# Performance work log

Hardware: AMD Instinct MI355X
Metric: run time of the kernel (lower is better)

## Reference

```python
import jax, jax.numpy as jnp
import numpy as np

D_MODEL = 1024
N_HEADS = 16
HEAD_DIM = D_MODEL // N_HEADS


def setup_inputs() -> dict:
    key = jax.random.key(0)
    k_x, k_q, k_k, k_v = jax.random.split(key, 4)
    B, S = 2, 2048
    x = jax.random.normal(k_x, (B, S, D_MODEL), dtype=jnp.float32)
    # nn.Linear weights stored as [out, in]; we apply x @ W.T
    scale = 1.0 / np.sqrt(D_MODEL)
    W_q = jax.random.uniform(k_q, (D_MODEL, D_MODEL), jnp.float32, -scale, scale)
    W_k = jax.random.uniform(k_k, (D_MODEL, D_MODEL), jnp.float32, -scale, scale)
    W_v = jax.random.uniform(k_v, (D_MODEL, D_MODEL), jnp.float32, -scale, scale)
    return {"x": x, "W_q": W_q, "W_k": W_k, "W_v": W_v}


def reference(x, W_q, W_k, W_v):
    B, S, D = x.shape
    H, Hd = N_HEADS, HEAD_DIM
    # QKV projections (Linear with no bias): x @ W.T
    Q = (x @ W_q.T).reshape(B, S, H, Hd).transpose(0, 2, 1, 3)  # [B,H,S,Hd]
    K = (x @ W_k.T).reshape(B, S, H, Hd).transpose(0, 2, 1, 3)
    V = (x @ W_v.T).reshape(B, S, H, Hd).transpose(0, 2, 1, 3)
    scores = jnp.einsum("bhqd,bhkd->bhqk", Q, K) / jnp.sqrt(jnp.float32(Hd))
    attn = jax.nn.softmax(scores, axis=-1)
    out = jnp.einsum("bhqk,bhkd->bhqd", attn, V)  # [B,H,S,Hd]
    return out.transpose(0, 2, 1, 3).reshape(B, S, H * Hd)
```

## Files before the change

### kernel.cpp

```cpp
#include <hip/hip_runtime.h>
#include <stdint.h>


typedef __bf16 bf16x8 __attribute__((ext_vector_type(8)));
typedef __bf16 bf16x4 __attribute__((ext_vector_type(4)));
typedef __bf16 bf16x2 __attribute__((ext_vector_type(2)));
typedef float  f32x2  __attribute__((ext_vector_type(2)));
typedef float  f32x4  __attribute__((ext_vector_type(4)));
typedef float  f32x16 __attribute__((ext_vector_type(16)));

#define D_MODEL 1024
#define SEQ     2048
#define NHEAD   16
#define HDIM    64
#define BS      4096

__device__ __forceinline__ void load_lds16(const void* g, void* lds) {
  __builtin_amdgcn_global_load_lds(
      (__attribute__((address_space(1))) void*)(uintptr_t)g,
      (__attribute__((address_space(3))) void*)(uintptr_t)lds,
      16, 0, 0);
}

#if __has_builtin(__builtin_amdgcn_exp2f)
#define EXP2F(x) __builtin_amdgcn_exp2f(x)
#else
#define EXP2F(x) __expf(0.6931471805599453f * (x))
#endif

__device__ __forceinline__ uint32_t pack_bf16_pair(float a, float b) {
  f32x2 f = {a, b};
  union { bf16x2 h; uint32_t u; } r;
  r.h = __builtin_convertvector(f, bf16x2);
  return r.u;
}

#define NX4 1048576
#define NW4 262144
__global__ void cvt_all(const float* __restrict__ x,  const float* __restrict__ wq,
                        const float* __restrict__ wk, const float* __restrict__ wv,
                        __bf16* __restrict__ xb,  __bf16* __restrict__ wqb,
                        __bf16* __restrict__ wkb, __bf16* __restrict__ wvb) {
  int i = blockIdx.x * blockDim.x + threadIdx.x;
  const float* in; __bf16* out; int j;
  if (i < NX4)                { in = x;  out = xb;  j = i; }
  else if (i < NX4 + NW4)     { in = wq; out = wqb; j = i - NX4; }
  else if (i < NX4 + 2*NW4)   { in = wk; out = wkb; j = i - NX4 - NW4; }
  else                        { in = wv; out = wvb; j = i - NX4 - 2*NW4; }
  float4 v = ((const float4*)in)[j];
  bf16x4 o;
  o[0] = (__bf16)v.x; o[1] = (__bf16)v.y;
  o[2] = (__bf16)v.z; o[3] = (__bf16)v.w;
  ((bf16x4*)out)[j] = o;
}

__global__ __launch_bounds__(256) void qkv_gemm(
    const __bf16* __restrict__ X,
    const __bf16* __restrict__ Wq, const __bf16* __restrict__ Wk,
    const __bf16* __restrict__ Wv,
    __bf16* __restrict__ Qb, __bf16* __restrict__ Kb, __bf16* __restrict__ Vt) {
  __shared__ __bf16 As[128 * 32];
  __shared__ __bf16 Bs[128 * 32];

  const __bf16* W = (blockIdx.z == 0) ? Wq : (blockIdx.z == 1) ? Wk : Wv;

  const int t    = threadIdx.x;
  const int wv   = t >> 6;
  const int lane = t & 63;
  const int l15  = lane & 15;
  const int quad = lane >> 4;
  const int m0   = blockIdx.y * 128;
  const int n0   = blockIdx.x * 128;
  const int wm   = (wv >> 1) * 64;
  const int wn   = (wv & 1) * 64;

  f32x4 acc[4][4] = {};

  for (int it = 0; it < 32; ++it) {
    const int k0 = it * 32;
#pragma unroll
    for (int p = 0; p < 2; ++p) {
      const int c   = p * 256 + t;
      const int row = c >> 2;
      const int ko  = (c & 3) * 8;
      const unsigned lb = (unsigned)((p * 256 + wv * 64) * 16);
      load_lds16(X + (size_t)(m0 + row) * D_MODEL + k0 + ko, (char*)As + lb);
      load_lds16(W + (size_t)(n0 + row) * D_MODEL + k0 + ko, (char*)Bs + lb);
    }
    __syncthreads();

    bf16x8 af[4], bfb[4];
#pragma unroll
    for (int i = 0; i < 4; ++i)
      af[i] = *(const bf16x8*)&As[(wm + i * 16 + l15) * 32 + quad * 8];
#pragma unroll
    for (int j = 0; j < 4; ++j)
      bfb[j] = *(const bf16x8*)&Bs[(wn + j * 16 + l15) * 32 + quad * 8];
#pragma unroll
    for (int i = 0; i < 4; ++i)
#pragma unroll
      for (int j = 0; j < 4; ++j)
        acc[i][j] = __builtin_amdgcn_mfma_f32_16x16x32_bf16(af[i], bfb[j],
                                                            acc[i][j], 0, 0, 0);
    __syncthreads();
  }

  if (blockIdx.z != 2) {
    __bf16* Out = (blockIdx.z == 0) ? Qb : Kb;
    const float qs = (blockIdx.z == 0) ? 0.125f * 1.4426950408889634f : 1.0f;
#pragma unroll
    for (int i = 0; i < 4; ++i) {
      const int rg = m0 + wm + i * 16 + quad * 4;
#pragma unroll
      for (int j = 0; j < 4; ++j) {
        const int cg = n0 + wn + j * 16 + l15;
#pragma unroll
        for (int r2 = 0; r2 < 4; ++r2)
          Out[(size_t)(rg + r2) * D_MODEL + cg] = (__bf16)(acc[i][j][r2] * qs);
      }
    }
  } else {
#pragma unroll
    for (int i = 0; i < 4; ++i) {
      const int mg = m0 + wm + i * 16 + quad * 4;
#pragma unroll
      for (int j = 0; j < 4; ++j) {
        const int ng = n0 + wn + j * 16 + l15;
        bf16x4 v;
#pragma unroll
        for (int r2 = 0; r2 < 4; ++r2) v[r2] = (__bf16)acc[i][j][r2];
        *(bf16x4*)&Vt[(size_t)ng * BS + mg] = v;
      }
    }
  }
}

__global__ __launch_bounds__(256) void attn(
    const __bf16* __restrict__ Qb, const __bf16* __restrict__ Kb,
    const __bf16* __restrict__ Vt, float* __restrict__ out) {
  __shared__ __align__(16) char smem[16896];
  __bf16* Ks = (__bf16*)smem;
  __bf16* Vs = (__bf16*)(smem + 8192);
  float*  cmb = (float*)smem;

  const int t     = threadIdx.x;
  const int wv    = t >> 6;
  const int qgrp  = wv >> 1;
  const int ktile = wv & 1;
  const int lane  = t & 63;
  const int l31   = lane & 31;
  const int half  = lane >> 5;
  const int h     = blockIdx.y;
  const size_t bo = (size_t)blockIdx.z * SEQ;
  const int q0    = blockIdx.x * 64 + qgrp * 32;
  const int hd0   = h * HDIM;

  bf16x8 qf[4];
#pragma unroll
  for (int c = 0; c < 4; ++c)
    qf[c] = *(const bf16x8*)&Qb[(bo + q0 + l31) * D_MODEL + hd0 + c * 16 + half * 8];

  f32x2 lsum2 = {0.f, 0.f};
  f32x16 o_acc[2] = {};

  const int srow = ktile * 32 + l31;

  for (int kt = 0; kt < SEQ / 64; ++kt) {
    const int n0 = kt * 64;
#pragma unroll
    for (int p = 0; p < 2; ++p) {
      const int c   = p * 256 + t;
      const int row = c >> 3;
      const int cc  = (c & 7) ^ (row & 7);
      const unsigned lb = (unsigned)((p * 256 + wv * 64) * 16);
      load_lds16(Kb + (bo + n0 + row) * D_MODEL + hd0 + cc * 8, (char*)Ks + lb);
      load_lds16(Vt + (size_t)(hd0 + row) * BS + bo + n0 + cc * 8, (char*)Vs + lb);
    }
    __syncthreads();

    f32x16 st = {};
#pragma unroll
    for (int c = 0; c < 4; ++c) {
      const int pc = (2 * c + half) ^ (srow & 7);
      bf16x8 kf = *(const bf16x8*)&Ks[(srow * 8 + pc) * 8];
      st = __builtin_amdgcn_mfma_f32_32x32x16_bf16(kf, qf[c], st, 0, 0, 0);
    }

    uint32_t pk[8];
#pragma unroll
    for (int i = 0; i < 8; ++i) {
      float e0 = EXP2F(st[2 * i]);
      float e1 = EXP2F(st[2 * i + 1]);
      f32x2 e = {e0, e1};
      lsum2 += e;
      pk[i] = pack_bf16_pair(e0, e1);
    }

#pragma unroll
    for (int kc = 0; kc < 2; ++kc) {
      auto r02 = __builtin_amdgcn_permlane32_swap(pk[kc * 4 + 0], pk[kc * 4 + 2],
                                                  false, false);
      auto r13 = __builtin_amdgcn_permlane32_swap(pk[kc * 4 + 1], pk[kc * 4 + 3],
                                                  false, false);
      union { uint32_t u[4]; bf16x8 v; } pf;
      pf.u[0] = r02[0]; pf.u[1] = r13[0];
      pf.u[2] = r02[1]; pf.u[3] = r13[1];
#pragma unroll
      for (int dt = 0; dt < 2; ++dt) {
        const int row = dt * 32 + l31;
        const int pc  = (ktile * 4 + kc * 2 + half) ^ (row & 7);
        bf16x8 vf = *(const bf16x8*)&Vs[(row * 8 + pc) * 8];
        o_acc[dt] = __builtin_amdgcn_mfma_f32_32x32x16_bf16(vf, pf.v,
                                                            o_acc[dt], 0, 0, 0);
      }
    }
    __syncthreads();
  }

  float lsum = lsum2[0] + lsum2[1];

  if (ktile == 1) {
    float* p = cmb + (size_t)(qgrp * 64 + lane) * 33;
#pragma unroll
    for (int dt = 0; dt < 2; ++dt)
#pragma unroll
      for (int g = 0; g < 16; ++g) p[dt * 16 + g] = o_acc[dt][g];
    p[32] = lsum;
  }
  __syncthreads();
  if (ktile == 0) {
    const float* p = cmb + (size_t)(qgrp * 64 + lane) * 33;
#pragma unroll
    for (int dt = 0; dt < 2; ++dt)
#pragma unroll
      for (int g = 0; g < 16; ++g) o_acc[dt][g] += p[dt * 16 + g];
    lsum += p[32];
    lsum += __shfl_xor(lsum, 32);
    const float inv = 1.f / lsum;

    const size_t orow = (bo + q0 + l31) * D_MODEL + hd0;
#pragma unroll
    for (int dt = 0; dt < 2; ++dt)
#pragma unroll
      for (int g = 0; g < 4; ++g) {
        float4 v = make_float4(o_acc[dt][4 * g + 0] * inv, o_acc[dt][4 * g + 1] * inv,
                               o_acc[dt][4 * g + 2] * inv, o_acc[dt][4 * g + 3] * inv);
        *(float4*)&out[orow + dt * 32 + g * 8 + half * 4] = v;
      }
  }
}

extern "C" void kernel_launch(void* const* d_in, const int* in_sizes, int n_in,
                              void* d_out, int out_size, void* d_ws, size_t ws_size,
                              hipStream_t stream) {
  const float* x  = (const float*)d_in[0];
  const float* Wq = (const float*)d_in[1];
  const float* Wk = (const float*)d_in[2];
  const float* Wv = (const float*)d_in[3];
  float* out = (float*)d_out;

  char* ws = (char*)d_ws;
  __bf16* xb  = (__bf16*)(ws);
  __bf16* wqb = (__bf16*)(ws + (8u  << 20));
  __bf16* wkb = (__bf16*)(ws + (10u << 20));
  __bf16* wvb = (__bf16*)(ws + (12u << 20));
  __bf16* Qbf = (__bf16*)(ws + (14u << 20));
  __bf16* Kbf = (__bf16*)(ws + (22u << 20));
  __bf16* Vt  = (__bf16*)(ws + (30u << 20));

  cvt_all<<<(NX4 + 3 * NW4) / 256, 256, 0, stream>>>(x, Wq, Wk, Wv,
                                                     xb, wqb, wkb, wvb);

  qkv_gemm<<<dim3(8, 32, 3), 256, 0, stream>>>(xb, wqb, wkb, wvb, Qbf, Kbf, Vt);

  attn<<<dim3(SEQ / 64, NHEAD, 2), 256, 0, stream>>>(Qbf, Kbf, Vt, out);
}
```

Baseline: 162.3 us.

## Double-buffer K/V tiles in LDS and raise wave priority around MFMAs

The attention loop now uses two LDS buffers, issuing the async global-to-LDS loads for the next K/V tile before computing on the current one, with one vmcnt-wait plus barrier per tile instead of two syncthreads. Address computation is hoisted out of the loop into precomputed per-thread pointers. s_setprio is raised around the MFMA sections to favour matrix issue. The cost is double the LDS footprint, which may lower occupancy, and the single barrier relies on vmcnt ordering being enough to avoid write-after-read hazards on the reused buffer.

```diff
diff --git a/kernel.cpp b/kernel.cpp
--- a/kernel.cpp
+++ b/kernel.cpp
@@ -135,13 +135,17 @@
   }
 }
 
+#define VMBAR do {                                         \
+    asm volatile("s_waitcnt vmcnt(0)" ::: "memory");       \
+    __builtin_amdgcn_s_barrier();                          \
+    asm volatile("" ::: "memory");                         \
+  } while (0)
+
 __global__ __launch_bounds__(256) void attn(
     const __bf16* __restrict__ Qb, const __bf16* __restrict__ Kb,
     const __bf16* __restrict__ Vt, float* __restrict__ out) {
-  __shared__ __align__(16) char smem[16896];
-  __bf16* Ks = (__bf16*)smem;
-  __bf16* Vs = (__bf16*)(smem + 8192);
-  float*  cmb = (float*)smem;
+  __shared__ __align__(16) char smem[32768];
+  float* cmb = (float*)smem;
 
   const int t     = threadIdx.x;
   const int wv    = t >> 6;
@@ -160,31 +164,44 @@
   for (int c = 0; c < 4; ++c)
     qf[c] = *(const bf16x8*)&Qb[(bo + q0 + l31) * D_MODEL + hd0 + c * 16 + half * 8];
 
+  const int row0 = t >> 3;
+  const int row1 = 32 + row0;
+  const int cc0  = (t & 7) ^ (row0 & 7);
+  const int cc1  = (t & 7) ^ (row1 & 7);
+  const __bf16* kp0 = Kb + (bo + row0) * D_MODEL + hd0 + cc0 * 8;
+  const __bf16* kp1 = Kb + (bo + row1) * D_MODEL + hd0 + cc1 * 8;
+  const __bf16* vp0 = Vt + (size_t)(hd0 + row0) * BS + bo + cc0 * 8;
+  const __bf16* vp1 = Vt + (size_t)(hd0 + row1) * BS + bo + cc1 * 8;
+  const unsigned lb0 = (unsigned)(wv * 1024);
+  const unsigned lb1 = (unsigned)(4096 + wv * 1024);
+
   f32x2 lsum2 = {0.f, 0.f};
   f32x16 o_acc[2] = {};
 
   const int srow = ktile * 32 + l31;
 
-  for (int kt = 0; kt < SEQ / 64; ++kt) {
-    const int n0 = kt * 64;
-#pragma unroll
-    for (int p = 0; p < 2; ++p) {
-      const int c   = p * 256 + t;
-      const int row = c >> 3;
-      const int cc  = (c & 7) ^ (row & 7);
-      const unsigned lb = (unsigned)((p * 256 + wv * 64) * 16);
-      load_lds16(Kb + (bo + n0 + row) * D_MODEL + hd0 + cc * 8, (char*)Ks + lb);
-      load_lds16(Vt + (size_t)(hd0 + row) * BS + bo + n0 + cc * 8, (char*)Vs + lb);
-    }
-    __syncthreads();
+  auto stage = [&](char* base, int kt) {
+    const size_t ko = (size_t)kt * (64 * D_MODEL);
+    const int    vo = kt * 64;
+    load_lds16(kp0 + ko, base + lb0);
+    load_lds16(kp1 + ko, base + lb1);
+    load_lds16(vp0 + vo, base + 8192 + lb0);
+    load_lds16(vp1 + vo, base + 8192 + lb1);
+  };
+
+  auto tile_compute = [&](const char* base) {
+    const __bf16* Ks = (const __bf16*)base;
+    const __bf16* Vs = (const __bf16*)(base + 8192);
 
     f32x16 st = {};
+    __builtin_amdgcn_s_setprio(1);
 #pragma unroll
     for (int c = 0; c < 4; ++c) {
       const int pc = (2 * c + half) ^ (srow & 7);
       bf16x8 kf = *(const bf16x8*)&Ks[(srow * 8 + pc) * 8];
       st = __builtin_amdgcn_mfma_f32_32x32x16_bf16(kf, qf[c], st, 0, 0, 0);
     }
+    __builtin_amdgcn_s_setprio(0);
 
     uint32_t pk[8];
 #pragma unroll
@@ -196,6 +213,7 @@
       pk[i] = pack_bf16_pair(e0, e1);
     }
 
+    __builtin_amdgcn_s_setprio(1);
 #pragma unroll
     for (int kc = 0; kc < 2; ++kc) {
       auto r02 = __builtin_amdgcn_permlane32_swap(pk[kc * 4 + 0], pk[kc * 4 + 2],
@@ -214,7 +232,22 @@
                                                             o_acc[dt], 0, 0, 0);
       }
     }
-    __syncthreads();
+    __builtin_amdgcn_s_setprio(0);
+  };
+
+  char* const b0 = smem;
+  char* const b1 = smem + 16384;
+
+  stage(b0, 0);
+  VMBAR;
+
+  for (int kt2 = 0; kt2 < 16; ++kt2) {
+    stage(b1, 2 * kt2 + 1);
+    tile_compute(b0);
+    VMBAR;
+    if (kt2 < 15) stage(b0, 2 * kt2 + 2);
+    tile_compute(b1);
+    VMBAR;
   }
 
   float lsum = lsum2[0] + lsum2[1];
```

New measurement: 162.6 us. No clear change (+0.2%).

## Load K/V fragments directly into registers with double buffering instead of LDS

Applied to the files above, without the earlier changes.

The attention loop no longer stages K and V tiles through shared memory with global_load_lds and two barriers per iteration. Each wave now loads its own K and V MFMA fragments straight from global memory into registers, double-buffered across key tiles so the next tile's loads overlap the current tile's compute. It also raises wave priority with s_setprio around the MFMA blocks. The cost is more registers and more global/L2 traffic, because waves sharing a key tile no longer share the loaded data, and global reads of Vt fragments may be less coalesced.

```diff
diff --git a/kernel.cpp b/kernel.cpp
--- a/kernel.cpp
+++ b/kernel.cpp
@@ -138,10 +138,7 @@
 __global__ __launch_bounds__(256) void attn(
     const __bf16* __restrict__ Qb, const __bf16* __restrict__ Kb,
     const __bf16* __restrict__ Vt, float* __restrict__ out) {
-  __shared__ __align__(16) char smem[16896];
-  __bf16* Ks = (__bf16*)smem;
-  __bf16* Vs = (__bf16*)(smem + 8192);
-  float*  cmb = (float*)smem;
+  __shared__ __align__(16) float cmb[2 * 64 * 33];
 
   const int t     = threadIdx.x;
   const int wv    = t >> 6;
@@ -160,31 +157,33 @@
   for (int c = 0; c < 4; ++c)
     qf[c] = *(const bf16x8*)&Qb[(bo + q0 + l31) * D_MODEL + hd0 + c * 16 + half * 8];
 
+  const int srow = ktile * 32 + l31;
+  const __bf16* kP = Kb + (bo + srow) * D_MODEL + hd0 + half * 8;
+  const __bf16* vP = Vt + (size_t)(hd0 + l31) * BS + bo + ktile * 32 + half * 8;
+
   f32x2 lsum2 = {0.f, 0.f};
   f32x16 o_acc[2] = {};
 
-  const int srow = ktile * 32 + l31;
-
-  for (int kt = 0; kt < SEQ / 64; ++kt) {
-    const int n0 = kt * 64;
-#pragma unroll
-    for (int p = 0; p < 2; ++p) {
-      const int c   = p * 256 + t;
-      const int row = c >> 3;
-      const int cc  = (c & 7) ^ (row & 7);
-      const unsigned lb = (unsigned)((p * 256 + wv * 64) * 16);
-      load_lds16(Kb + (bo + n0 + row) * D_MODEL + hd0 + cc * 8, (char*)Ks + lb);
-      load_lds16(Vt + (size_t)(hd0 + row) * BS + bo + n0 + cc * 8, (char*)Vs + lb);
-    }
-    __syncthreads();
-
+  auto loadt = [&](bf16x8 (&kf)[4], bf16x8 (&vf)[4], int tt) {
+    const __bf16* kp = kP + (size_t)tt * (64 * D_MODEL);
+    const __bf16* vp = vP + tt * 64;
+#pragma unroll
+    for (int c = 0; c < 4; ++c)
+      kf[c] = *(const bf16x8*)(kp + c * 16);
+#pragma unroll
+    for (int kc = 0; kc < 2; ++kc)
+#pragma unroll
+      for (int dt = 0; dt < 2; ++dt)
+        vf[kc * 2 + dt] = *(const bf16x8*)(vp + (size_t)dt * (32 * BS) + kc * 16);
+  };
+
+  auto compute = [&](const bf16x8 (&kf)[4], const bf16x8 (&vf)[4]) {
     f32x16 st = {};
-#pragma unroll
-    for (int c = 0; c < 4; ++c) {
-      const int pc = (2 * c + half) ^ (srow & 7);
-      bf16x8 kf = *(const bf16x8*)&Ks[(srow * 8 + pc) * 8];
-      st = __builtin_amdgcn_mfma_f32_32x32x16_bf16(kf, qf[c], st, 0, 0, 0);
-    }
+    __builtin_amdgcn_s_setprio(1);
+#pragma unroll
+    for (int c = 0; c < 4; ++c)
+      st = __builtin_amdgcn_mfma_f32_32x32x16_bf16(kf[c], qf[c], st, 0, 0, 0);
+    __builtin_amdgcn_s_setprio(0);
 
     uint32_t pk[8];
 #pragma unroll
@@ -196,6 +195,7 @@
       pk[i] = pack_bf16_pair(e0, e1);
     }
 
+    __builtin_amdgcn_s_setprio(1);
 #pragma unroll
     for (int kc = 0; kc < 2; ++kc) {
       auto r02 = __builtin_amdgcn_permlane32_swap(pk[kc * 4 + 0], pk[kc * 4 + 2],
@@ -206,15 +206,20 @@
       pf.u[0] = r02[0]; pf.u[1] = r13[0];
       pf.u[2] = r02[1]; pf.u[3] = r13[1];
 #pragma unroll
-      for (int dt = 0; dt < 2; ++dt) {
-        const int row = dt * 32 + l31;
-        const int pc  = (ktile * 4 + kc * 2 + half) ^ (row & 7);
-        bf16x8 vf = *(const bf16x8*)&Vs[(row * 8 + pc) * 8];
-        o_acc[dt] = __builtin_amdgcn_mfma_f32_32x32x16_bf16(vf, pf.v,
+      for (int dt = 0; dt < 2; ++dt)
+        o_acc[dt] = __builtin_amdgcn_mfma_f32_32x32x16_bf16(vf[kc * 2 + dt], pf.v,
                                                             o_acc[dt], 0, 0, 0);
-      }
-    }
-    __syncthreads();
+    }
+    __builtin_amdgcn_s_setprio(0);
+  };
+
+  bf16x8 ka[4], va[4], kb_[4], vb_[4];
+  loadt(ka, va, 0);
+  for (int kt = 0; kt < 32; kt += 2) {
+    loadt(kb_, vb_, kt + 1);
+    compute(ka, va);
+    if (kt + 2 < 32) loadt(ka, va, kt + 2);
+    compute(kb_, vb_);
   }
 
   float lsum = lsum2[0] + lsum2[1];
```

Result: slower. 228.3 us (+40.7%).

## Split attention KV sweep across four waves per query group with 128-key tiles

Applied to the files above, without the earlier changes.

The attention kernel now launches 512 threads, so each 32-query group is served by four waves that each take a 32-key slice of a 128-key tile, instead of two waves over a 64-key tile. This halves the number of outer-loop iterations and barriers and amortizes the LDS staging over more keys, with precomputed load addresses. In exchange it doubles shared memory per block and adds a two-stage tree reduction of partial outputs across the waves at the end. Higher thread count with a launch-bound hint of 8 may constrain registers.

```diff
diff --git a/kernel.cpp b/kernel.cpp
--- a/kernel.cpp
+++ b/kernel.cpp
@@ -135,18 +135,18 @@
   }
 }
 
-__global__ __launch_bounds__(256) void attn(
+__global__ __launch_bounds__(512, 8) void attn(
     const __bf16* __restrict__ Qb, const __bf16* __restrict__ Kb,
     const __bf16* __restrict__ Vt, float* __restrict__ out) {
-  __shared__ __align__(16) char smem[16896];
+  __shared__ __align__(16) char smem[33792];
   __bf16* Ks = (__bf16*)smem;
-  __bf16* Vs = (__bf16*)(smem + 8192);
+  __bf16* Vs = (__bf16*)(smem + 16384);
   float*  cmb = (float*)smem;
 
   const int t     = threadIdx.x;
   const int wv    = t >> 6;
-  const int qgrp  = wv >> 1;
-  const int ktile = wv & 1;
+  const int qgrp  = wv >> 2;
+  const int ktile = wv & 3;
   const int lane  = t & 63;
   const int l31   = lane & 31;
   const int half  = lane >> 5;
@@ -160,22 +160,28 @@
   for (int c = 0; c < 4; ++c)
     qf[c] = *(const bf16x8*)&Qb[(bo + q0 + l31) * D_MODEL + hd0 + c * 16 + half * 8];
 
+  const int rK = t >> 3;
+  const int cK = (t & 7) ^ (rK & 7);
+  const int rV = t >> 4;
+  const int cV = (t & 15) ^ (rV & 15);
+  const __bf16* kSrc = Kb + (bo + rK) * D_MODEL + hd0 + cK * 8;
+  const __bf16* vSrc = Vt + (size_t)(hd0 + rV) * BS + bo + cV * 8;
+  char* const kDst0 = smem + wv * 1024;
+  char* const kDst1 = smem + 8192 + wv * 1024;
+  char* const vDst0 = smem + 16384 + wv * 1024;
+  char* const vDst1 = smem + 16384 + 8192 + wv * 1024;
+
   f32x2 lsum2 = {0.f, 0.f};
   f32x16 o_acc[2] = {};
 
   const int srow = ktile * 32 + l31;
 
-  for (int kt = 0; kt < SEQ / 64; ++kt) {
-    const int n0 = kt * 64;
-#pragma unroll
-    for (int p = 0; p < 2; ++p) {
-      const int c   = p * 256 + t;
-      const int row = c >> 3;
-      const int cc  = (c & 7) ^ (row & 7);
-      const unsigned lb = (unsigned)((p * 256 + wv * 64) * 16);
-      load_lds16(Kb + (bo + n0 + row) * D_MODEL + hd0 + cc * 8, (char*)Ks + lb);
-      load_lds16(Vt + (size_t)(hd0 + row) * BS + bo + n0 + cc * 8, (char*)Vs + lb);
-    }
+  for (int kt = 0; kt < SEQ / 128; ++kt) {
+    const int n0 = kt * 128;
+    load_lds16(kSrc + (size_t)n0 * D_MODEL, kDst0);
+    load_lds16(kSrc + (size_t)(n0 + 64) * D_MODEL, kDst1);
+    load_lds16(vSrc + n0, vDst0);
+    load_lds16(vSrc + (size_t)32 * BS + n0, vDst1);
     __syncthreads();
 
     f32x16 st = {};
@@ -208,8 +214,8 @@
 #pragma unroll
       for (int dt = 0; dt < 2; ++dt) {
         const int row = dt * 32 + l31;
-        const int pc  = (ktile * 4 + kc * 2 + half) ^ (row & 7);
-        bf16x8 vf = *(const bf16x8*)&Vs[(row * 8 + pc) * 8];
+        const int pc  = (ktile * 4 + kc * 2 + half) ^ (row & 15);
+        bf16x8 vf = *(const bf16x8*)&Vs[(row * 16 + pc) * 8];
         o_acc[dt] = __builtin_amdgcn_mfma_f32_32x32x16_bf16(vf, pf.v,
                                                             o_acc[dt], 0, 0, 0);
       }
@@ -219,8 +225,32 @@
 
   float lsum = lsum2[0] + lsum2[1];
 
-  if (ktile == 1) {
-    float* p = cmb + (size_t)(qgrp * 64 + lane) * 33;
+  const int slotA = qgrp * 2;
+  const int slotB = qgrp * 2 + 1;
+  {
+    const int ws = (ktile == 1) ? slotA : slotB;
+    if (ktile == 1 || ktile == 3) {
+      float* p = cmb + (size_t)(ws * 64 + lane) * 33;
+#pragma unroll
+      for (int dt = 0; dt < 2; ++dt)
+#pragma unroll
+        for (int g = 0; g < 16; ++g) p[dt * 16 + g] = o_acc[dt][g];
+      p[32] = lsum;
+    }
+  }
+  __syncthreads();
+  if (ktile == 0 || ktile == 2) {
+    const int rs = (ktile == 0) ? slotA : slotB;
+    const float* p = cmb + (size_t)(rs * 64 + lane) * 33;
+#pragma unroll
+    for (int dt = 0; dt < 2; ++dt)
+#pragma unroll
+      for (int g = 0; g < 16; ++g) o_acc[dt][g] += p[dt * 16 + g];
+    lsum += p[32];
+  }
+  __syncthreads();
+  if (ktile == 2) {
+    float* p = cmb + (size_t)(slotA * 64 + lane) * 33;
 #pragma unroll
     for (int dt = 0; dt < 2; ++dt)
 #pragma unroll
@@ -229,7 +259,7 @@
   }
   __syncthreads();
   if (ktile == 0) {
-    const float* p = cmb + (size_t)(qgrp * 64 + lane) * 33;
+    const float* p = cmb + (size_t)(slotA * 64 + lane) * 33;
 #pragma unroll
     for (int dt = 0; dt < 2; ++dt)
 #pragma unroll
@@ -273,5 +303,5 @@
 
   qkv_gemm<<<dim3(8, 32, 3), 256, 0, stream>>>(xb, wqb, wkb, wvb, Qbf, Kbf, Vt);
 
-  attn<<<dim3(SEQ / 64, NHEAD, 2), 256, 0, stream>>>(Qbf, Kbf, Vt, out);
-}
+  attn<<<dim3(SEQ / 64, NHEAD, 2), 512, 0, stream>>>(Qbf, Kbf, Vt, out);
+}
```

Result: slower. 491.0 us (+202.6%).
